# Kernel optimization log

Hardware: AMD Instinct MI355X
Metric: run time of the kernel (lower is better)

The kernel has to match this reference:

```python
import jax, jax.numpy as jnp
import numpy as np

B, S, D, H = 2, 2048, 1024, 16
DEPTH = D // H

def setup_inputs() -> dict:
    key = jax.random.key(0)
    ks = jax.random.split(key, 6)
    sc = 0.02
    return {
        "x": jax.random.normal(ks[0], (B, S, D), dtype=jnp.float32),
        "mask": jnp.ones((S, S), dtype=jnp.int32),
        "wq": jax.random.normal(ks[1], (D, D), dtype=jnp.float32) * sc,
        "bq": jnp.zeros((D,), dtype=jnp.float32),
        "wk": jax.random.normal(ks[2], (D, D), dtype=jnp.float32) * sc,
        "bk": jnp.zeros((D,), dtype=jnp.float32),
        "wv": jax.random.normal(ks[3], (D, D), dtype=jnp.float32) * sc,
        "bv": jnp.zeros((D,), dtype=jnp.float32),
        "wo": jax.random.normal(ks[4], (D, D), dtype=jnp.float32) * sc,
        "bo": jnp.zeros((D,), dtype=jnp.float32),
    }

def _split_heads(t):
    # [B,S,D] -> [B,H,S,depth]
    b, s, _ = t.shape
    return t.reshape(b, s, H, DEPTH).transpose(0, 2, 1, 3)

def reference(x, mask, wq, bq, wk, bk, wv, bv, wo, bo):
    q = _split_heads(x @ wq + bq)
    k = _split_heads(x @ wk + bk)
    v = _split_heads(x @ wv + bv)
    scale = 1.0 / jnp.sqrt(jnp.asarray(DEPTH, x.dtype))
    scores = jnp.einsum('bhqd,bhkd->bhqk', q, k) * scale
    # Faithful to original: band_part(ones,-1,0) is the LOWER triangle
    # (incl. diagonal), and it is ADDED times -1e9 -> lower triangle masked.
    s_len = mask.shape[0]
    tri = jnp.tril(jnp.ones((s_len, s_len), dtype=x.dtype))
    scores = scores + tri * (-1e9)
    attn = jax.nn.softmax(scores, axis=-1)  # dropout is identity at inference
    out = jnp.einsum('bhqk,bhkd->bhqd', attn, v)
    out = out.transpose(0, 2, 1, 3).reshape(x.shape[0], -1, D)
    return out @ wo + bo
```

## Files before the change

### kernel.cpp

```cpp
#include <hip/hip_runtime.h>
#include <hip/hip_bf16.h>


using bf16   = __bf16;
using bf16x2 = __attribute__((ext_vector_type(2))) __bf16;
using bf16x4 = __attribute__((ext_vector_type(4))) __bf16;
using bf16x8 = __attribute__((ext_vector_type(8))) __bf16;
using f32x4  = __attribute__((ext_vector_type(4))) float;
using uintx2 = __attribute__((ext_vector_type(2))) unsigned int;
using uintx4 = __attribute__((ext_vector_type(4))) unsigned int;

#define ATTN_LOG2E 1.4426950408889634f
#define ATTN_MBIAS (-11.541560327111707f)

__device__ __forceinline__ void load_lds16(const void* g, void* l) {
  __builtin_amdgcn_global_load_lds(
      (const __attribute__((address_space(1))) void*)g,
      (__attribute__((address_space(3))) void*)l, 16, 0, 0);
}

__device__ __forceinline__ unsigned int packbf(float a, float b) {
  bf16x2 v;
  v[0] = (bf16)a;
  v[1] = (bf16)b;
  return __builtin_bit_cast(unsigned int, v);
}

__device__ __forceinline__ void xchg_p(unsigned int u, unsigned int v, int hi,
                                       unsigned int& f, unsigned int& s) {
#if __has_builtin(__builtin_amdgcn_permlane32_swap) && \
    __has_builtin(__builtin_amdgcn_permlane16_swap)
  uintx2 ab = __builtin_amdgcn_permlane32_swap(u, v, false, false);
  uintx2 fs = __builtin_amdgcn_permlane16_swap(ab[0], ab[1], false, false);
  f = fs[0];
  s = fs[1];
#else
  unsigned int a = (hi < 2) ? u : (unsigned int)__shfl_xor((int)v, 32);
  unsigned int b = (hi < 2) ? (unsigned int)__shfl_xor((int)u, 32) : v;
  unsigned int a16 = (unsigned int)__shfl_xor((int)a, 16);
  unsigned int b16 = (unsigned int)__shfl_xor((int)b, 16);
  f = (hi & 1) ? b16 : a;
  s = (hi & 1) ? b : a16;
#endif
}

__global__ __launch_bounds__(256) void prep_kernel(
    const float* __restrict__ x, bf16* __restrict__ xb,
    const float* __restrict__ wq, const float* __restrict__ wk,
    const float* __restrict__ wv, const float* __restrict__ wo,
    bf16* __restrict__ wT) {
  const int t = threadIdx.x;
  int bid = blockIdx.x;
  if (bid < 4096) {
    const int i = (bid * 256 + t) * 4;
    const float4 v = *(const float4*)(x + i);
    bf16x4 o;
    o[0] = (bf16)v.x; o[1] = (bf16)v.y; o[2] = (bf16)v.z; o[3] = (bf16)v.w;
    *(bf16x4*)(xb + i) = o;
    return;
  }
  bid -= 4096;
  const int sel = bid >> 8;
  const float* w = (sel == 0) ? wq : (sel == 1) ? wk : (sel == 2) ? wv : wo;
  bf16* out = wT + (size_t)sel * 1048576;
  __shared__ float tile[64][65];
  const int n0 = (bid & 15) * 64;
  const int k0 = ((bid >> 4) & 15) * 64;
#pragma unroll
  for (int p = 0; p < 4; ++p) {
    const int row = p * 16 + (t >> 4);
    const int c4  = (t & 15) * 4;
    const float4 v = *(const float4*)&w[(size_t)(k0 + row) * 1024 + n0 + c4];
    tile[row][c4 + 0] = v.x; tile[row][c4 + 1] = v.y;
    tile[row][c4 + 2] = v.z; tile[row][c4 + 3] = v.w;
  }
  __syncthreads();
#pragma unroll
  for (int p = 0; p < 4; ++p) {
    const int rn = p * 16 + (t >> 4);
    const int c4 = (t & 15) * 4;
    bf16x4 o;
#pragma unroll
    for (int j = 0; j < 4; ++j) o[j] = (bf16)tile[c4 + j][rn];
    *(bf16x4*)&out[(size_t)(n0 + rn) * 1024 + k0 + c4] = o;
  }
}

template <int MODE>
__global__ __launch_bounds__(256, 2) void gemm_bt(
    const bf16* __restrict__ A, const bf16* __restrict__ Bt,
    const float* __restrict__ bias0, const float* __restrict__ bias1,
    const float* __restrict__ bias2, bf16* __restrict__ qf,
    bf16* __restrict__ kfr, bf16* __restrict__ vfr, float* __restrict__ fout,
    int Nblocks) {
  __shared__ __align__(16) char smem[32768];
  char* sA = smem;
  char* sB = smem + 16384;
  const int tid = threadIdx.x;
  const int lane = tid & 63;
  const int w = tid >> 6;
  const int wm = w >> 1, wn = w & 1;
  const int bid = blockIdx.x;
  const int m0 = (bid / Nblocks) * 128;
  const int n0 = (bid % Nblocks) * 128;

  const char* Ab = (const char*)A;
  const char* Bb = (const char*)Bt;
  size_t srcA[4], srcB[4];
#pragma unroll
  for (int it = 0; it < 4; ++it) {
    const int o = it * 4096 + tid * 16;
    const int r = o >> 7;
    const int cg = ((o >> 4) & 7) ^ (r & 7);
    srcA[it] = (size_t)(m0 + r) * 2048 + cg * 16;
    srcB[it] = (size_t)(n0 + r) * 2048 + cg * 16;
  }

  f32x4 acc[4][4] = {};

  for (int kt = 0; kt < 16; ++kt) {
    const size_t kb = (size_t)kt * 128;
#pragma unroll
    for (int it = 0; it < 4; ++it) {
      load_lds16(Ab + srcA[it] + kb, sA + it * 4096 + w * 1024);
      load_lds16(Bb + srcB[it] + kb, sB + it * 4096 + w * 1024);
    }
    asm volatile("s_waitcnt vmcnt(0)" ::: "memory");
    __syncthreads();
#pragma unroll
    for (int ks = 0; ks < 2; ++ks) {
      bf16x8 aF[4], bF[4];
      const int g = (lane >> 4) + 4 * ks;
#pragma unroll
      for (int i = 0; i < 4; ++i) {
        const int ra = wm * 64 + i * 16 + (lane & 15);
        aF[i] = *(const bf16x8*)(sA + ra * 128 + ((g ^ (ra & 7)) << 4));
        const int rb = wn * 64 + i * 16 + (lane & 15);
        bF[i] = *(const bf16x8*)(sB + rb * 128 + ((g ^ (rb & 7)) << 4));
      }
#pragma unroll
      for (int mi = 0; mi < 4; ++mi)
#pragma unroll
        for (int ni = 0; ni < 4; ++ni)
          acc[mi][ni] = __builtin_amdgcn_mfma_f32_16x16x32_bf16(
              aF[mi], bF[ni], acc[mi][ni], 0, 0, 0);
    }
    __syncthreads();
  }

  const int cn = lane & 15;
  const int gq = lane >> 4;
#pragma unroll
  for (int mi = 0; mi < 4; ++mi) {
#pragma unroll
    for (int ni = 0; ni < 4; ++ni) {
      const int n  = n0 + wn * 64 + ni * 16 + cn;
      const int mb = m0 + wm * 64 + mi * 16 + 4 * gq;
      const f32x4 v = acc[mi][ni];
      if (MODE == 0) {
        const float bias =
            (n < 1024) ? bias0[n] : ((n < 2048) ? bias1[n - 1024] : bias2[n - 2048]);
        if (n < 1024) {
#pragma unroll
          for (int j = 0; j < 4; ++j)
            qf[(size_t)(mb + j) * 1024 + n] = (bf16)(v[j] + bias);
        } else if (n < 2048) {
          const int dg = n - 1024;
          const int hh = dg >> 6, d = dg & 63;
          const int ks = d >> 5, hl = (d >> 3) & 3, e = d & 7;
          const int bb = mb >> 11, sl = mb & 2047;
          const int ktt = sl >> 6, tt = (sl >> 4) & 3, ql = sl & 15;
          bf16* dst = kfr +
                      ((((size_t)(bb * 16 + hh) * 32 + ktt) * 4 + tt) * 2 + ks) *
                          512 +
                      (hl * 16 + ql) * 8 + e;
#pragma unroll
          for (int j = 0; j < 4; ++j) dst[j * 8] = (bf16)(v[j] + bias);
        } else {
          const int dg = n - 2048;
          const int hh = dg >> 6, d = dg & 63;
          const int dt = d >> 4, dc = d & 15;
          const int bb = mb >> 11, sl = mb & 2047;
          const int ktt = sl >> 6, ks = (sl >> 5) & 1, hl = (sl >> 3) & 3,
                    e0 = sl & 7;
          bf16x4 pk;
#pragma unroll
          for (int j = 0; j < 4; ++j) pk[j] = (bf16)(v[j] + bias);
          *(bf16x4*)(vfr +
                     ((((size_t)(bb * 16 + hh) * 32 + ktt) * 4 + dt) * 2 + ks) *
                         512 +
                     (hl * 16 + dc) * 8 + e0) = pk;
        }
      } else {
        const float bias = bias0[n];
#pragma unroll
        for (int j = 0; j < 4; ++j)
          fout[(size_t)(mb + j) * 1024 + n] = v[j] + bias;
      }
    }
  }
}

__global__ __launch_bounds__(256, 2) void attn_kernel(
    const bf16* __restrict__ qf, const bf16* __restrict__ kfr,
    const bf16* __restrict__ vfr, bf16* __restrict__ ao,
    bf16* __restrict__ o2buf, float* __restrict__ lbuf) {
  const int tid  = threadIdx.x;
  const int lane = tid & 63;
  const int hi   = lane >> 4;
  const int qlo  = lane & 15;
  const int w    = tid >> 6;
  const int u  = blockIdx.x >> 5;
  const int bh = blockIdx.x & 31;
  const int b = bh >> 4, h = bh & 15;

  const char* kfb = (const char*)kfr + (size_t)bh * 262144 + lane * 16;
  const char* vfb = (const char*)vfr + (size_t)bh * 262144 + lane * 16;
  const char* qbb = (const char*)qf + ((size_t)b * 2048) * 2048 + h * 128;

  bf16x8 onesB;
#pragma unroll
  for (int i = 0; i < 8; ++i) onesB[i] = (bf16)1.0f;

  int nseg, sjq[2], skb[2], ske[2], smode[2];
  if (u < 8) {
    nseg = 1;
    sjq[0] = u; skb[0] = 2 * u; ske[0] = 2 * u + 17; smode[0] = 1;
    sjq[1] = 0; skb[1] = 0; ske[1] = 0; smode[1] = 0;
  } else {
    const int j = u - 8;
    nseg = 2;
    sjq[0] = j;      skb[0] = 2 * j + 17; ske[0] = 32; smode[0] = 2;
    sjq[1] = 15 - j; skb[1] = 30 - 2 * j; ske[1] = 32; smode[1] = 0;
  }

  for (int seg = 0; seg < nseg; ++seg) {
    const int jq = sjq[seg], kbeg = skb[seg], kend = ske[seg];
    const int mode = smode[seg];

    const int q0 = jq * 128;
    const int qb = q0 + w * 32;

    bf16x8 qA[2][2];
#pragma unroll
    for (int nt = 0; nt < 2; ++nt) {
      const char* qrow = qbb + (size_t)(qb + 16 * nt + qlo) * 2048;
#pragma unroll
      for (int ks = 0; ks < 2; ++ks) {
        qA[nt][ks] = *(const bf16x8*)(qrow + ks * 64 + hi * 16);
#pragma unroll
        for (int i = 0; i < 8; ++i)
          qA[nt][ks][i] = (bf16)(0.125f * (float)qA[nt][ks][i]);
      }
    }

    f32x4 lacc[2] = {};
    f32x4 O[2][4] = {};

    bf16x8 kA[2][4], kB[2][4], vF[2][4];

    auto LOADK = [&](int kt, bf16x8 (&kd)[2][4]) {
      const char* kT = kfb + (size_t)kt * 8192;
#pragma unroll
      for (int ks = 0; ks < 2; ++ks)
#pragma unroll
        for (int t = 0; t < 4; ++t)
          kd[ks][t] = *(const bf16x8*)(kT + (t * 2 + ks) * 1024);
    };
    auto LOADV = [&](int kt) {
      const char* vT = vfb + (size_t)kt * 8192;
#pragma unroll
      for (int ks = 0; ks < 2; ++ks)
#pragma unroll
        for (int dt = 0; dt < 4; ++dt)
          vF[ks][dt] = *(const bf16x8*)(vT + (dt * 2 + ks) * 1024);
    };

    auto COMPUTE = [&](int kt, bf16x8 (&kFr)[2][4]) {
      f32x4 sc[2][4] = {};
#pragma unroll
      for (int ks = 0; ks < 2; ++ks)
#pragma unroll
        for (int t = 0; t < 4; ++t) {
          sc[0][t] = __builtin_amdgcn_mfma_f32_16x16x32_bf16(
              kFr[ks][t], qA[0][ks], sc[0][t], 0, 0, 0);
          sc[1][t] = __builtin_amdgcn_mfma_f32_16x16x32_bf16(
              kFr[ks][t], qA[1][ks], sc[1][t], 0, 0, 0);
        }

      if (kt * 64 < q0 + 128) {
        const int k0t = kt * 64;
#pragma unroll
        for (int nt = 0; nt < 2; ++nt)
#pragma unroll
          for (int t = 0; t < 4; ++t)
#pragma unroll
            for (int j = 0; j < 4; ++j) {
              const int kk = k0t + t * 16 + 4 * hi + j;
              const int qq = qb + 16 * nt + qlo;
              if (kk <= qq) sc[nt][t][j] = -1e30f;
            }
      }

#pragma unroll
      for (int nt = 0; nt < 2; ++nt) {
        unsigned int W[4][2];
#pragma unroll
        for (int t = 0; t < 4; ++t)
#pragma unroll
          for (int p = 0; p < 2; ++p)
            W[t][p] = packbf(
                exp2f(fmaf(sc[nt][t][2 * p], ATTN_LOG2E, ATTN_MBIAS)),
                exp2f(fmaf(sc[nt][t][2 * p + 1], ATTN_LOG2E, ATTN_MBIAS)));
#pragma unroll
        for (int ks = 0; ks < 2; ++ks) {
          uintx4 w4;
#pragma unroll
          for (int p = 0; p < 2; ++p) {
            unsigned int f, s;
            xchg_p(W[2 * ks][p], W[2 * ks + 1][p], hi, f, s);
            w4[p] = f;
            w4[2 + p] = s;
          }
          const bf16x8 pA = __builtin_bit_cast(bf16x8, w4);
          lacc[nt] = __builtin_amdgcn_mfma_f32_16x16x32_bf16(pA, onesB,
                                                             lacc[nt], 0, 0, 0);
#pragma unroll
          for (int dt = 0; dt < 4; ++dt)
            O[nt][dt] = __builtin_amdgcn_mfma_f32_16x16x32_bf16(
                pA, vF[ks][dt], O[nt][dt], 0, 0, 0);
        }
      }
    };

    LOADK(kbeg, kA);
    for (int kt = kbeg; kt < kend; kt += 2) {
      LOADV(kt);
      if (kt + 1 < kend) LOADK(kt + 1, kB);
      COMPUTE(kt, kA);
      if (kt + 1 < kend) {
        LOADV(kt + 1);
        if (kt + 2 < kend) LOADK(kt + 2, kA);
        COMPUTE(kt + 1, kB);
      }
    }

    if (mode == 0) {
#pragma unroll
      for (int nt = 0; nt < 2; ++nt)
#pragma unroll
        for (int j = 0; j < 4; ++j) {
          const float linv = (lacc[nt][j] > 0.f) ? 1.f / lacc[nt][j] : 0.f;
          const int qg = qb + 16 * nt + 4 * hi + j;
#pragma unroll
          for (int dt = 0; dt < 4; ++dt)
            ao[(size_t)(b * 2048 + qg) * 1024 + h * 64 + dt * 16 + qlo] =
                (bf16)(O[nt][dt][j] * linv);
        }
    } else {
      const int qtbh = jq * 32 + bh;
      const int slot = mode - 1;
#pragma unroll
      for (int nt = 0; nt < 2; ++nt)
#pragma unroll
        for (int j = 0; j < 4; ++j) {
          const int r = w * 32 + 16 * nt + 4 * hi + j;
#pragma unroll
          for (int dt = 0; dt < 4; ++dt) {
            const bf16 vv = (bf16)O[nt][dt][j];
            if (mode == 1)
              ao[(size_t)(b * 2048 + q0 + r) * 1024 + h * 64 + dt * 16 + qlo] =
                  vv;
            else
              o2buf[(size_t)(qtbh * 128 + r) * 64 + dt * 16 + qlo] = vv;
          }
        }
      if (qlo == 0) {
#pragma unroll
        for (int nt = 0; nt < 2; ++nt)
#pragma unroll
          for (int j = 0; j < 4; ++j)
            lbuf[(qtbh * 2 + slot) * 128 + (w * 32 + 16 * nt + 4 * hi + j)] =
                lacc[nt][j];
      }
    }
  }
}

__global__ __launch_bounds__(256) void combine_kernel(
    const bf16* __restrict__ o2buf, const float* __restrict__ lbuf,
    const bf16* __restrict__ vfr, bf16* __restrict__ ao) {
  const int bid = blockIdx.x;
  if (bid >= 256) {
    const int tid = threadIdx.x;
    const int lane = tid & 63, w = tid >> 6;
    const int gw = (bid - 256) * 4 + w;
    const int bh = gw >> 2, dt = gw & 3;
    const int b = bh >> 4, h = bh & 15;
    const char* vfb = (const char*)vfr + (size_t)bh * 262144 + lane * 16;
    float s = 0.f;
    for (int kt = 0; kt < 32; ++kt) {
#pragma unroll
      for (int ks = 0; ks < 2; ++ks) {
        const bf16x8 v =
            *(const bf16x8*)(vfb + (size_t)kt * 8192 + (dt * 2 + ks) * 1024);
#pragma unroll
        for (int e = 0; e < 8; ++e) s += (float)v[e];
      }
    }
    s += __shfl_xor(s, 16);
    s += __shfl_xor(s, 32);
    if ((lane >> 4) == 0)
      ao[(size_t)(b * 2048 + 2047) * 1024 + h * 64 + dt * 16 + lane] =
          (bf16)(s * (1.f / 2048.f));
    return;
  }

  const int qtbh = bid;
  const int jq = qtbh >> 5, bh = qtbh & 31;
  const int b = bh >> 4, h = bh & 15;
  const int t = threadIdx.x;
  const int r = t >> 1;
  const int c0 = (t & 1) * 32;

  const float l1 = lbuf[(qtbh * 2 + 0) * 128 + r];
  const float l2 = lbuf[(qtbh * 2 + 1) * 128 + r];
  const float denom = l1 + l2;
  const float linv = (denom > 0.f) ? 1.f / denom : 0.f;

  bf16* arow = ao + ((size_t)(b * 2048 + jq * 128 + r) * 1024 + h * 64 + c0);
  const bf16* o2row = o2buf + ((size_t)(qtbh * 128 + r) * 64 + c0);
#pragma unroll
  for (int i = 0; i < 4; ++i) {
    const bf16x8 o1 = *(const bf16x8*)(arow + i * 8);
    const bf16x8 o2 = *(const bf16x8*)(o2row + i * 8);
    bf16x8 o;
#pragma unroll
    for (int j = 0; j < 8; ++j)
      o[j] = (bf16)(((float)o1[j] + (float)o2[j]) * linv);
    *(bf16x8*)(arow + i * 8) = o;
  }
}

extern "C" void kernel_launch(void* const* d_in, const int* in_sizes, int n_in,
                              void* d_out, int out_size, void* d_ws,
                              size_t ws_size, hipStream_t stream) {
  const float* x  = (const float*)d_in[0];
  const float* wq = (const float*)d_in[2];
  const float* bq = (const float*)d_in[3];
  const float* wk = (const float*)d_in[4];
  const float* bk = (const float*)d_in[5];
  const float* wv = (const float*)d_in[6];
  const float* bv = (const float*)d_in[7];
  const float* wo = (const float*)d_in[8];
  const float* bo = (const float*)d_in[9];
  float* out = (float*)d_out;

  if (ws_size < (size_t)25165824 * 2) return;

  bf16* ws    = (bf16*)d_ws;
  bf16* xb    = ws;
  bf16* wqkvT = xb + 4194304;
  bf16* woT   = wqkvT + 3145728;
  bf16* qfp   = woT + 1048576;
  bf16* kfrag = qfp + 4194304;
  bf16* vfrag = kfrag + 4194304;
  bf16* aop   = vfrag + 4194304;

  bf16*  o2buf = xb;
  float* lbuf  = (float*)(xb + 2097152);

  prep_kernel<<<5120, 256, 0, stream>>>(x, xb, wq, wk, wv, wo, wqkvT);

  gemm_bt<0><<<32 * 24, 256, 0, stream>>>(xb, wqkvT, bq, bk, bv, qfp, kfrag,
                                          vfrag, nullptr, 24);
  attn_kernel<<<512, 256, 0, stream>>>(qfp, kfrag, vfrag, aop, o2buf, lbuf);
  combine_kernel<<<288, 256, 0, stream>>>(o2buf, lbuf, vfrag, aop);
  gemm_bt<1><<<32 * 8, 256, 0, stream>>>(aop, woT, bo, nullptr, nullptr, nullptr,
                                         nullptr, nullptr, out, 8);
}
```

Baseline: 108.7 us.

## Split attention key range across two wave groups and reduce through LDS

The attention kernel now runs 512 threads per block: two groups of four waves each process half of the key tiles for the same query rows. The second group writes its partial O and row-sum accumulators to shared memory, and the first group adds them before doing the existing output and partial-result writes. This doubles the parallelism per query tile to hide latency and improve occupancy. In exchange it drops the software double-buffered K/V prefetch, adds a block-wide barrier and an LDS round-trip, and tightens the register budget through the new launch bounds.

```diff
diff --git a/kernel.cpp b/kernel.cpp
--- a/kernel.cpp
+++ b/kernel.cpp
@@ -201,15 +201,19 @@
   }
 }
 
-__global__ __launch_bounds__(256, 2) void attn_kernel(
+__global__ __launch_bounds__(512, 4) void attn_kernel(
     const bf16* __restrict__ qf, const bf16* __restrict__ kfr,
     const bf16* __restrict__ vfr, bf16* __restrict__ ao,
     bf16* __restrict__ o2buf, float* __restrict__ lbuf) {
+  __shared__ __align__(16) char smem[40960];
+
   const int tid  = threadIdx.x;
   const int lane = tid & 63;
   const int hi   = lane >> 4;
   const int qlo  = lane & 15;
-  const int w    = tid >> 6;
+  const int wave = tid >> 6;
+  const int wg   = wave >> 2;
+  const int w    = wave & 3;
   const int u  = blockIdx.x >> 5;
   const int bh = blockIdx.x & 31;
   const int b = bh >> 4, h = bh & 15;
@@ -234,6 +238,8 @@
     sjq[1] = 15 - j; skb[1] = 30 - 2 * j; ske[1] = 32; smode[1] = 0;
   }
 
+  char* const lbase = smem + w * 10240 + lane * 160;
+
   for (int seg = 0; seg < nseg; ++seg) {
     const int jq = sjq[seg], kbeg = skb[seg], kend = ske[seg];
     const int mode = smode[seg];
@@ -257,26 +263,25 @@
     f32x4 lacc[2] = {};
     f32x4 O[2][4] = {};
 
-    bf16x8 kA[2][4], kB[2][4], vF[2][4];
-
-    auto LOADK = [&](int kt, bf16x8 (&kd)[2][4]) {
+    const int half0 = (kend - kbeg + 1) >> 1;
+    const int myb = wg ? (kbeg + half0) : kbeg;
+    const int mye = wg ? kend : (kbeg + half0);
+
+    for (int kt = myb; kt < mye; ++kt) {
       const char* kT = kfb + (size_t)kt * 8192;
+      const char* vT = vfb + (size_t)kt * 8192;
+      bf16x8 kFr[2][4], vF[2][4];
 #pragma unroll
       for (int ks = 0; ks < 2; ++ks)
 #pragma unroll
         for (int t = 0; t < 4; ++t)
-          kd[ks][t] = *(const bf16x8*)(kT + (t * 2 + ks) * 1024);
-    };
-    auto LOADV = [&](int kt) {
-      const char* vT = vfb + (size_t)kt * 8192;
+          kFr[ks][t] = *(const bf16x8*)(kT + (t * 2 + ks) * 1024);
 #pragma unroll
       for (int ks = 0; ks < 2; ++ks)
 #pragma unroll
         for (int dt = 0; dt < 4; ++dt)
           vF[ks][dt] = *(const bf16x8*)(vT + (dt * 2 + ks) * 1024);
-    };
-
-    auto COMPUTE = [&](int kt, bf16x8 (&kFr)[2][4]) {
+
       f32x4 sc[2][4] = {};
 #pragma unroll
       for (int ks = 0; ks < 2; ++ks)
@@ -331,59 +336,76 @@
                 pA, vF[ks][dt], O[nt][dt], 0, 0, 0);
         }
       }
-    };
-
-    LOADK(kbeg, kA);
-    for (int kt = kbeg; kt < kend; kt += 2) {
-      LOADV(kt);
-      if (kt + 1 < kend) LOADK(kt + 1, kB);
-      COMPUTE(kt, kA);
-      if (kt + 1 < kend) {
-        LOADV(kt + 1);
-        if (kt + 2 < kend) LOADK(kt + 2, kA);
-        COMPUTE(kt + 1, kB);
-      }
-    }
-
-    if (mode == 0) {
+    }
+
+    if (wg == 1) {
 #pragma unroll
       for (int nt = 0; nt < 2; ++nt)
 #pragma unroll
-        for (int j = 0; j < 4; ++j) {
-          const float linv = (lacc[nt][j] > 0.f) ? 1.f / lacc[nt][j] : 0.f;
-          const int qg = qb + 16 * nt + 4 * hi + j;
-#pragma unroll
-          for (int dt = 0; dt < 4; ++dt)
-            ao[(size_t)(b * 2048 + qg) * 1024 + h * 64 + dt * 16 + qlo] =
-                (bf16)(O[nt][dt][j] * linv);
+        for (int dt = 0; dt < 4; ++dt)
+          *(f32x4*)(lbase + (nt * 4 + dt) * 16) = O[nt][dt];
+      *(f32x4*)(lbase + 128) = lacc[0];
+      *(f32x4*)(lbase + 144) = lacc[1];
+    }
+    __syncthreads();
+    if (wg == 0) {
+#pragma unroll
+      for (int nt = 0; nt < 2; ++nt)
+#pragma unroll
+        for (int dt = 0; dt < 4; ++dt) {
+          const f32x4 o1 = *(const f32x4*)(lbase + (nt * 4 + dt) * 16);
+#pragma unroll
+          for (int j = 0; j < 4; ++j) O[nt][dt][j] += o1[j];
         }
-    } else {
-      const int qtbh = jq * 32 + bh;
-      const int slot = mode - 1;
-#pragma unroll
-      for (int nt = 0; nt < 2; ++nt)
-#pragma unroll
-        for (int j = 0; j < 4; ++j) {
-          const int r = w * 32 + 16 * nt + 4 * hi + j;
-#pragma unroll
-          for (int dt = 0; dt < 4; ++dt) {
-            const bf16 vv = (bf16)O[nt][dt][j];
-            if (mode == 1)
-              ao[(size_t)(b * 2048 + q0 + r) * 1024 + h * 64 + dt * 16 + qlo] =
-                  vv;
-            else
-              o2buf[(size_t)(qtbh * 128 + r) * 64 + dt * 16 + qlo] = vv;
+      const f32x4 la0 = *(const f32x4*)(lbase + 128);
+      const f32x4 la1 = *(const f32x4*)(lbase + 144);
+#pragma unroll
+      for (int j = 0; j < 4; ++j) {
+        lacc[0][j] += la0[j];
+        lacc[1][j] += la1[j];
+      }
+
+      if (mode == 0) {
+#pragma unroll
+        for (int nt = 0; nt < 2; ++nt)
+#pragma unroll
+          for (int j = 0; j < 4; ++j) {
+            const float linv = (lacc[nt][j] > 0.f) ? 1.f / lacc[nt][j] : 0.f;
+            const int qg = qb + 16 * nt + 4 * hi + j;
+#pragma unroll
+            for (int dt = 0; dt < 4; ++dt)
+              ao[(size_t)(b * 2048 + qg) * 1024 + h * 64 + dt * 16 + qlo] =
+                  (bf16)(O[nt][dt][j] * linv);
           }
+      } else {
+        const int qtbh = jq * 32 + bh;
+        const int slot = mode - 1;
+#pragma unroll
+        for (int nt = 0; nt < 2; ++nt)
+#pragma unroll
+          for (int j = 0; j < 4; ++j) {
+            const int r = w * 32 + 16 * nt + 4 * hi + j;
+#pragma unroll
+            for (int dt = 0; dt < 4; ++dt) {
+              const bf16 vv = (bf16)O[nt][dt][j];
+              if (mode == 1)
+                ao[(size_t)(b * 2048 + q0 + r) * 1024 + h * 64 + dt * 16 +
+                   qlo] = vv;
+              else
+                o2buf[(size_t)(qtbh * 128 + r) * 64 + dt * 16 + qlo] = vv;
+            }
+          }
+        if (qlo == 0) {
+#pragma unroll
+          for (int nt = 0; nt < 2; ++nt)
+#pragma unroll
+            for (int j = 0; j < 4; ++j)
+              lbuf[(qtbh * 2 + slot) * 128 +
+                   (w * 32 + 16 * nt + 4 * hi + j)] = lacc[nt][j];
         }
-      if (qlo == 0) {
-#pragma unroll
-        for (int nt = 0; nt < 2; ++nt)
-#pragma unroll
-          for (int j = 0; j < 4; ++j)
-            lbuf[(qtbh * 2 + slot) * 128 + (w * 32 + 16 * nt + 4 * hi + j)] =
-                lacc[nt][j];
-      }
-    }
+      }
+    }
+    __syncthreads();
   }
 }
 
@@ -474,7 +496,7 @@
 
   gemm_bt<0><<<32 * 24, 256, 0, stream>>>(xb, wqkvT, bq, bk, bv, qfp, kfrag,
                                           vfrag, nullptr, 24);
-  attn_kernel<<<512, 256, 0, stream>>>(qfp, kfrag, vfrag, aop, o2buf, lbuf);
+  attn_kernel<<<512, 512, 0, stream>>>(qfp, kfrag, vfrag, aop, o2buf, lbuf);
   combine_kernel<<<288, 256, 0, stream>>>(o2buf, lbuf, vfrag, aop);
   gemm_bt<1><<<32 * 8, 256, 0, stream>>>(aop, woT, bo, nullptr, nullptr, nullptr,
                                          nullptr, nullptr, out, 8);
```

After: 142.3 us. 1.31x slower.

## Rewrite QKV projection GEMM with 256x256 tiles, double-buffered LDS and XOR swizzle

Applied to the files above, without the earlier changes.

Replaces the templated 128x128 QKV GEMM with a dedicated kernel using 512 threads, 256x256 output tiles, a BK=64 double-buffered LDS pipeline via global_load_lds, and an XOR-swizzled LDS layout. Block indices are remapped so neighbouring blocks share operand tiles. The larger tiles raise arithmetic intensity and cut redundant global loads, and the prefetch overlaps loads with MFMA work. In exchange it uses 128KB of LDS and many accumulator registers, and launches only 192 blocks, which may leave some of the 256 compute units idle.

```diff
diff --git a/kernel.cpp b/kernel.cpp
--- a/kernel.cpp
+++ b/kernel.cpp
@@ -86,13 +86,148 @@
   }
 }
 
-template <int MODE>
-__global__ __launch_bounds__(256, 2) void gemm_bt(
+__global__ __launch_bounds__(512, 2) void gemm_qkv(
     const bf16* __restrict__ A, const bf16* __restrict__ Bt,
     const float* __restrict__ bias0, const float* __restrict__ bias1,
     const float* __restrict__ bias2, bf16* __restrict__ qf,
-    bf16* __restrict__ kfr, bf16* __restrict__ vfr, float* __restrict__ fout,
-    int Nblocks) {
+    bf16* __restrict__ kfr, bf16* __restrict__ vfr) {
+  __shared__ __align__(16) char smem[131072];
+  char* const sAb = smem;
+  char* const sBb = smem + 65536;
+
+  const int tid  = threadIdx.x;
+  const int lane = tid & 63;
+  const int qlo  = lane & 15;
+  const int hi   = lane >> 4;
+  const int wv   = tid >> 6;
+  const int wm   = wv >> 2;
+  const int wn   = wv & 3;
+
+  const int swz = (blockIdx.x & 7) * 24 + (blockIdx.x >> 3);
+  const int m0 = (swz / 12) * 256;
+  const int n0 = (swz % 12) * 256;
+
+  const char* Ab = (const char*)A;
+  const char* Bb = (const char*)Bt;
+
+  const int r_  = tid >> 3;
+  const int cg_ = (tid & 7) ^ (r_ & 7);
+  size_t srcA[4], srcB[4];
+#pragma unroll
+  for (int i = 0; i < 4; ++i) {
+    srcA[i] = (size_t)(m0 + i * 64 + r_) * 2048 + cg_ * 16;
+    srcB[i] = (size_t)(n0 + i * 64 + r_) * 2048 + cg_ * 16;
+  }
+
+  f32x4 acc[8][4] = {};
+
+  auto STAGE = [&](int kt, int buf) {
+    const size_t kb = (size_t)kt * 128;
+    char* dA = sAb + buf * 32768 + wv * 1024;
+    char* dB = sBb + buf * 32768 + wv * 1024;
+#pragma unroll
+    for (int i = 0; i < 4; ++i) {
+      load_lds16(Ab + srcA[i] + kb, dA + i * 8192);
+      load_lds16(Bb + srcB[i] + kb, dB + i * 8192);
+    }
+  };
+
+  STAGE(0, 0);
+  asm volatile("s_waitcnt vmcnt(0)" ::: "memory");
+  __syncthreads();
+
+  for (int kt = 0; kt < 16; ++kt) {
+    const int cur = kt & 1;
+    if (kt + 1 < 16) STAGE(kt + 1, cur ^ 1);
+
+    const char* bA = sAb + cur * 32768;
+    const char* bB = sBb + cur * 32768;
+
+    bf16x8 bF[4][2];
+#pragma unroll
+    for (int ni = 0; ni < 4; ++ni)
+#pragma unroll
+      for (int kk = 0; kk < 2; ++kk) {
+        const int rb = wn * 64 + ni * 16 + qlo;
+        const int g = kk * 4 + hi;
+        bF[ni][kk] = *(const bf16x8*)(bB + rb * 128 + ((g ^ (rb & 7)) << 4));
+      }
+
+#pragma unroll
+    for (int half = 0; half < 2; ++half) {
+      bf16x8 aF[4][2];
+#pragma unroll
+      for (int mi2 = 0; mi2 < 4; ++mi2)
+#pragma unroll
+        for (int kk = 0; kk < 2; ++kk) {
+          const int ra = wm * 128 + (half * 4 + mi2) * 16 + qlo;
+          const int g = kk * 4 + hi;
+          aF[mi2][kk] =
+              *(const bf16x8*)(bA + ra * 128 + ((g ^ (ra & 7)) << 4));
+        }
+#pragma unroll
+      for (int mi2 = 0; mi2 < 4; ++mi2)
+#pragma unroll
+        for (int ni = 0; ni < 4; ++ni)
+#pragma unroll
+          for (int kk = 0; kk < 2; ++kk)
+            acc[half * 4 + mi2][ni] = __builtin_amdgcn_mfma_f32_16x16x32_bf16(
+                aF[mi2][kk], bF[ni][kk], acc[half * 4 + mi2][ni], 0, 0, 0);
+    }
+
+    if (kt + 1 < 16) {
+      asm volatile("s_waitcnt vmcnt(0)" ::: "memory");
+      __syncthreads();
+    }
+  }
+
+#pragma unroll
+  for (int mi = 0; mi < 8; ++mi) {
+#pragma unroll
+    for (int ni = 0; ni < 4; ++ni) {
+      const int n  = n0 + wn * 64 + ni * 16 + qlo;
+      const int mb = m0 + wm * 128 + mi * 16 + 4 * hi;
+      const f32x4 v = acc[mi][ni];
+      const float bias =
+          (n < 1024) ? bias0[n] : ((n < 2048) ? bias1[n - 1024] : bias2[n - 2048]);
+      if (n < 1024) {
+#pragma unroll
+        for (int j = 0; j < 4; ++j)
+          qf[(size_t)(mb + j) * 1024 + n] = (bf16)(v[j] + bias);
+      } else if (n < 2048) {
+        const int dg = n - 1024;
+        const int hh = dg >> 6, d = dg & 63;
+        const int ks = d >> 5, hl = (d >> 3) & 3, e = d & 7;
+        const int bb = mb >> 11, sl = mb & 2047;
+        const int ktt = sl >> 6, tt = (sl >> 4) & 3, ql = sl & 15;
+        bf16* dst = kfr +
+                    ((((size_t)(bb * 16 + hh) * 32 + ktt) * 4 + tt) * 2 + ks) *
+                        512 +
+                    (hl * 16 + ql) * 8 + e;
+#pragma unroll
+        for (int j = 0; j < 4; ++j) dst[j * 8] = (bf16)(v[j] + bias);
+      } else {
+        const int dg = n - 2048;
+        const int hh = dg >> 6, d = dg & 63;
+        const int dt = d >> 4, dc = d & 15;
+        const int bb = mb >> 11, sl = mb & 2047;
+        const int ktt = sl >> 6, ks = (sl >> 5) & 1, hl = (sl >> 3) & 3,
+                  e0 = sl & 7;
+        bf16x4 pk;
+#pragma unroll
+        for (int j = 0; j < 4; ++j) pk[j] = (bf16)(v[j] + bias);
+        *(bf16x4*)(vfr +
+                   ((((size_t)(bb * 16 + hh) * 32 + ktt) * 4 + dt) * 2 + ks) *
+                       512 +
+                   (hl * 16 + dc) * 8 + e0) = pk;
+      }
+    }
+  }
+}
+
+__global__ __launch_bounds__(256, 2) void gemm_out(
+    const bf16* __restrict__ A, const bf16* __restrict__ Bt,
+    const float* __restrict__ bias0, float* __restrict__ fout, int Nblocks) {
   __shared__ __align__(16) char smem[32768];
   char* sA = smem;
   char* sB = smem + 16384;
@@ -157,46 +292,10 @@
       const int n  = n0 + wn * 64 + ni * 16 + cn;
       const int mb = m0 + wm * 64 + mi * 16 + 4 * gq;
       const f32x4 v = acc[mi][ni];
-      if (MODE == 0) {
-        const float bias =
-            (n < 1024) ? bias0[n] : ((n < 2048) ? bias1[n - 1024] : bias2[n - 2048]);
-        if (n < 1024) {
-#pragma unroll
-          for (int j = 0; j < 4; ++j)
-            qf[(size_t)(mb + j) * 1024 + n] = (bf16)(v[j] + bias);
-        } else if (n < 2048) {
-          const int dg = n - 1024;
-          const int hh = dg >> 6, d = dg & 63;
-          const int ks = d >> 5, hl = (d >> 3) & 3, e = d & 7;
-          const int bb = mb >> 11, sl = mb & 2047;
-          const int ktt = sl >> 6, tt = (sl >> 4) & 3, ql = sl & 15;
-          bf16* dst = kfr +
-                      ((((size_t)(bb * 16 + hh) * 32 + ktt) * 4 + tt) * 2 + ks) *
-                          512 +
-                      (hl * 16 + ql) * 8 + e;
-#pragma unroll
-          for (int j = 0; j < 4; ++j) dst[j * 8] = (bf16)(v[j] + bias);
-        } else {
-          const int dg = n - 2048;
-          const int hh = dg >> 6, d = dg & 63;
-          const int dt = d >> 4, dc = d & 15;
-          const int bb = mb >> 11, sl = mb & 2047;
-          const int ktt = sl >> 6, ks = (sl >> 5) & 1, hl = (sl >> 3) & 3,
-                    e0 = sl & 7;
-          bf16x4 pk;
-#pragma unroll
-          for (int j = 0; j < 4; ++j) pk[j] = (bf16)(v[j] + bias);
-          *(bf16x4*)(vfr +
-                     ((((size_t)(bb * 16 + hh) * 32 + ktt) * 4 + dt) * 2 + ks) *
-                         512 +
-                     (hl * 16 + dc) * 8 + e0) = pk;
-        }
-      } else {
-        const float bias = bias0[n];
-#pragma unroll
-        for (int j = 0; j < 4; ++j)
-          fout[(size_t)(mb + j) * 1024 + n] = v[j] + bias;
-      }
+      const float bias = bias0[n];
+#pragma unroll
+      for (int j = 0; j < 4; ++j)
+        fout[(size_t)(mb + j) * 1024 + n] = v[j] + bias;
     }
   }
 }
@@ -472,10 +571,8 @@
 
   prep_kernel<<<5120, 256, 0, stream>>>(x, xb, wq, wk, wv, wo, wqkvT);
 
-  gemm_bt<0><<<32 * 24, 256, 0, stream>>>(xb, wqkvT, bq, bk, bv, qfp, kfrag,
-                                          vfrag, nullptr, 24);
+  gemm_qkv<<<192, 512, 0, stream>>>(xb, wqkvT, bq, bk, bv, qfp, kfrag, vfrag);
   attn_kernel<<<512, 256, 0, stream>>>(qfp, kfrag, vfrag, aop, o2buf, lbuf);
   combine_kernel<<<288, 256, 0, stream>>>(o2buf, lbuf, vfrag, aop);
-  gemm_bt<1><<<32 * 8, 256, 0, stream>>>(aop, woT, bo, nullptr, nullptr, nullptr,
-                                         nullptr, nullptr, out, 8);
-}
+  gemm_out<<<32 * 8, 256, 0, stream>>>(aop, woT, bo, out, 8);
+}
```

Measured after the change: 111.6 us. 1.03x slower.

## Split attention key ranges into table-driven chunks across more blocks

Applied to the files above, without the earlier changes.

Replaces the two-segment-per-block causal work split with a 36-entry chunk table, so each of 1152 blocks handles one query tile over a bounded key range (up to three partial slots per tile, combined later). This aims to balance work across CUs and raise the block count. Occupancy bounds go from 2 to 4 blocks per CU, and the manual double-buffered K prefetch is dropped in favour of a simple load-then-compute loop. In exchange the combine kernel reads three partial buffers for some tiles, and the lost prefetch may expose load latency.

```diff
diff --git a/kernel.cpp b/kernel.cpp
--- a/kernel.cpp
+++ b/kernel.cpp
@@ -43,6 +43,44 @@
   s = (hi & 1) ? b : a16;
 #endif
 }
+
+__device__ const unsigned int kChunkTab[36] = {
+    0u  | (0u << 8)  | (11u << 16) | (0u << 24),
+    0u  | (11u << 8) | (22u << 16) | (1u << 24),
+    0u  | (22u << 8) | (32u << 16) | (2u << 24),
+    1u  | (2u << 8)  | (12u << 16) | (0u << 24),
+    1u  | (12u << 8) | (22u << 16) | (1u << 24),
+    1u  | (22u << 8) | (32u << 16) | (2u << 24),
+    2u  | (4u << 8)  | (14u << 16) | (0u << 24),
+    2u  | (14u << 8) | (23u << 16) | (1u << 24),
+    2u  | (23u << 8) | (32u << 16) | (2u << 24),
+    3u  | (6u << 8)  | (15u << 16) | (0u << 24),
+    3u  | (15u << 8) | (24u << 16) | (1u << 24),
+    4u  | (8u << 8)  | (16u << 16) | (0u << 24),
+    4u  | (16u << 8) | (24u << 16) | (1u << 24),
+    4u  | (24u << 8) | (32u << 16) | (2u << 24),
+    8u  | (16u << 8) | (24u << 16) | (0u << 24),
+    8u  | (24u << 8) | (32u << 16) | (1u << 24),
+    12u | (24u << 8) | (32u << 16) | (3u << 24),
+    3u  | (24u << 8) | (32u << 16) | (2u << 24),
+    5u  | (10u << 8) | (18u << 16) | (0u << 24),
+    5u  | (18u << 8) | (25u << 16) | (1u << 24),
+    5u  | (25u << 8) | (32u << 16) | (2u << 24),
+    6u  | (12u << 8) | (19u << 16) | (0u << 24),
+    6u  | (19u << 8) | (26u << 16) | (1u << 24),
+    9u  | (18u << 8) | (25u << 16) | (0u << 24),
+    9u  | (25u << 8) | (32u << 16) | (1u << 24),
+    6u  | (26u << 8) | (32u << 16) | (2u << 24),
+    7u  | (14u << 8) | (20u << 16) | (0u << 24),
+    7u  | (20u << 8) | (26u << 16) | (1u << 24),
+    7u  | (26u << 8) | (32u << 16) | (2u << 24),
+    10u | (20u << 8) | (26u << 16) | (0u << 24),
+    10u | (26u << 8) | (32u << 16) | (1u << 24),
+    13u | (26u << 8) | (32u << 16) | (3u << 24),
+    11u | (22u << 8) | (27u << 16) | (0u << 24),
+    11u | (27u << 8) | (32u << 16) | (1u << 24),
+    14u | (28u << 8) | (32u << 16) | (3u << 24),
+    15u | (30u << 8) | (32u << 16) | (3u << 24)};
 
 __global__ __launch_bounds__(256) void prep_kernel(
     const float* __restrict__ x, bf16* __restrict__ xb,
@@ -201,10 +239,11 @@
   }
 }
 
-__global__ __launch_bounds__(256, 2) void attn_kernel(
+__global__ __launch_bounds__(256, 4) void attn_kernel(
     const bf16* __restrict__ qf, const bf16* __restrict__ kfr,
     const bf16* __restrict__ vfr, bf16* __restrict__ ao,
-    bf16* __restrict__ o2buf, float* __restrict__ lbuf) {
+    bf16* __restrict__ sc1, bf16* __restrict__ sc2,
+    float* __restrict__ lbuf) {
   const int tid  = threadIdx.x;
   const int lane = tid & 63;
   const int hi   = lane >> 4;
@@ -214,6 +253,10 @@
   const int bh = blockIdx.x & 31;
   const int b = bh >> 4, h = bh & 15;
 
+  const unsigned int ent = kChunkTab[u];
+  const int jq = ent & 255, kbeg = (ent >> 8) & 255, kend = (ent >> 16) & 255;
+  const int slot = ent >> 24;
+
   const char* kfb = (const char*)kfr + (size_t)bh * 262144 + lane * 16;
   const char* vfb = (const char*)vfr + (size_t)bh * 262144 + lane * 16;
   const char* qbb = (const char*)qf + ((size_t)b * 2048) * 2048 + h * 128;
@@ -222,179 +265,147 @@
 #pragma unroll
   for (int i = 0; i < 8; ++i) onesB[i] = (bf16)1.0f;
 
-  int nseg, sjq[2], skb[2], ske[2], smode[2];
-  if (u < 8) {
-    nseg = 1;
-    sjq[0] = u; skb[0] = 2 * u; ske[0] = 2 * u + 17; smode[0] = 1;
-    sjq[1] = 0; skb[1] = 0; ske[1] = 0; smode[1] = 0;
+  const int q0 = jq * 128;
+  const int qb = q0 + w * 32;
+
+  bf16x8 qA[2][2];
+#pragma unroll
+  for (int nt = 0; nt < 2; ++nt) {
+    const char* qrow = qbb + (size_t)(qb + 16 * nt + qlo) * 2048;
+#pragma unroll
+    for (int ks = 0; ks < 2; ++ks) {
+      qA[nt][ks] = *(const bf16x8*)(qrow + ks * 64 + hi * 16);
+#pragma unroll
+      for (int i = 0; i < 8; ++i)
+        qA[nt][ks][i] = (bf16)(0.125f * (float)qA[nt][ks][i]);
+    }
+  }
+
+  f32x4 lacc[2] = {};
+  f32x4 O[2][4] = {};
+
+  for (int kt = kbeg; kt < kend; ++kt) {
+    const char* kT = kfb + (size_t)kt * 8192;
+    const char* vT = vfb + (size_t)kt * 8192;
+    bf16x8 kFr[2][4], vF[2][4];
+#pragma unroll
+    for (int ks = 0; ks < 2; ++ks)
+#pragma unroll
+      for (int t = 0; t < 4; ++t)
+        kFr[ks][t] = *(const bf16x8*)(kT + (t * 2 + ks) * 1024);
+#pragma unroll
+    for (int ks = 0; ks < 2; ++ks)
+#pragma unroll
+      for (int dt = 0; dt < 4; ++dt)
+        vF[ks][dt] = *(const bf16x8*)(vT + (dt * 2 + ks) * 1024);
+
+    f32x4 sc[2][4] = {};
+#pragma unroll
+    for (int ks = 0; ks < 2; ++ks)
+#pragma unroll
+      for (int t = 0; t < 4; ++t) {
+        sc[0][t] = __builtin_amdgcn_mfma_f32_16x16x32_bf16(
+            kFr[ks][t], qA[0][ks], sc[0][t], 0, 0, 0);
+        sc[1][t] = __builtin_amdgcn_mfma_f32_16x16x32_bf16(
+            kFr[ks][t], qA[1][ks], sc[1][t], 0, 0, 0);
+      }
+
+    if (kt * 64 < q0 + 128) {
+      const int k0t = kt * 64;
+#pragma unroll
+      for (int nt = 0; nt < 2; ++nt)
+#pragma unroll
+        for (int t = 0; t < 4; ++t)
+#pragma unroll
+          for (int j = 0; j < 4; ++j) {
+            const int kk = k0t + t * 16 + 4 * hi + j;
+            const int qq = qb + 16 * nt + qlo;
+            if (kk <= qq) sc[nt][t][j] = -1e30f;
+          }
+    }
+
+#pragma unroll
+    for (int nt = 0; nt < 2; ++nt) {
+      unsigned int W[4][2];
+#pragma unroll
+      for (int t = 0; t < 4; ++t)
+#pragma unroll
+        for (int p = 0; p < 2; ++p)
+          W[t][p] = packbf(
+              exp2f(fmaf(sc[nt][t][2 * p], ATTN_LOG2E, ATTN_MBIAS)),
+              exp2f(fmaf(sc[nt][t][2 * p + 1], ATTN_LOG2E, ATTN_MBIAS)));
+#pragma unroll
+      for (int ks = 0; ks < 2; ++ks) {
+        uintx4 w4;
+#pragma unroll
+        for (int p = 0; p < 2; ++p) {
+          unsigned int f, s;
+          xchg_p(W[2 * ks][p], W[2 * ks + 1][p], hi, f, s);
+          w4[p] = f;
+          w4[2 + p] = s;
+        }
+        const bf16x8 pA = __builtin_bit_cast(bf16x8, w4);
+        lacc[nt] = __builtin_amdgcn_mfma_f32_16x16x32_bf16(pA, onesB, lacc[nt],
+                                                           0, 0, 0);
+#pragma unroll
+        for (int dt = 0; dt < 4; ++dt)
+          O[nt][dt] = __builtin_amdgcn_mfma_f32_16x16x32_bf16(
+              pA, vF[ks][dt], O[nt][dt], 0, 0, 0);
+      }
+    }
+  }
+
+  if (slot == 3) {
+#pragma unroll
+    for (int nt = 0; nt < 2; ++nt)
+#pragma unroll
+      for (int j = 0; j < 4; ++j) {
+        const float linv = (lacc[nt][j] > 0.f) ? 1.f / lacc[nt][j] : 0.f;
+        const int qg = qb + 16 * nt + 4 * hi + j;
+#pragma unroll
+        for (int dt = 0; dt < 4; ++dt)
+          ao[(size_t)(b * 2048 + qg) * 1024 + h * 64 + dt * 16 + qlo] =
+              (bf16)(O[nt][dt][j] * linv);
+      }
   } else {
-    const int j = u - 8;
-    nseg = 2;
-    sjq[0] = j;      skb[0] = 2 * j + 17; ske[0] = 32; smode[0] = 2;
-    sjq[1] = 15 - j; skb[1] = 30 - 2 * j; ske[1] = 32; smode[1] = 0;
-  }
-
-  for (int seg = 0; seg < nseg; ++seg) {
-    const int jq = sjq[seg], kbeg = skb[seg], kend = ske[seg];
-    const int mode = smode[seg];
-
-    const int q0 = jq * 128;
-    const int qb = q0 + w * 32;
-
-    bf16x8 qA[2][2];
-#pragma unroll
-    for (int nt = 0; nt < 2; ++nt) {
-      const char* qrow = qbb + (size_t)(qb + 16 * nt + qlo) * 2048;
-#pragma unroll
-      for (int ks = 0; ks < 2; ++ks) {
-        qA[nt][ks] = *(const bf16x8*)(qrow + ks * 64 + hi * 16);
-#pragma unroll
-        for (int i = 0; i < 8; ++i)
-          qA[nt][ks][i] = (bf16)(0.125f * (float)qA[nt][ks][i]);
-      }
-    }
-
-    f32x4 lacc[2] = {};
-    f32x4 O[2][4] = {};
-
-    bf16x8 kA[2][4], kB[2][4], vF[2][4];
-
-    auto LOADK = [&](int kt, bf16x8 (&kd)[2][4]) {
-      const char* kT = kfb + (size_t)kt * 8192;
-#pragma unroll
-      for (int ks = 0; ks < 2; ++ks)
-#pragma unroll
-        for (int t = 0; t < 4; ++t)
-          kd[ks][t] = *(const bf16x8*)(kT + (t * 2 + ks) * 1024);
-    };
-    auto LOADV = [&](int kt) {
-      const char* vT = vfb + (size_t)kt * 8192;
-#pragma unroll
-      for (int ks = 0; ks < 2; ++ks)
-#pragma unroll
-        for (int dt = 0; dt < 4; ++dt)
-          vF[ks][dt] = *(const bf16x8*)(vT + (dt * 2 + ks) * 1024);
-    };
-
-    auto COMPUTE = [&](int kt, bf16x8 (&kFr)[2][4]) {
-      f32x4 sc[2][4] = {};
-#pragma unroll
-      for (int ks = 0; ks < 2; ++ks)
-#pragma unroll
-        for (int t = 0; t < 4; ++t) {
-          sc[0][t] = __builtin_amdgcn_mfma_f32_16x16x32_bf16(
-              kFr[ks][t], qA[0][ks], sc[0][t], 0, 0, 0);
-          sc[1][t] = __builtin_amdgcn_mfma_f32_16x16x32_bf16(
-              kFr[ks][t], qA[1][ks], sc[1][t], 0, 0, 0);
-        }
-
-      if (kt * 64 < q0 + 128) {
-        const int k0t = kt * 64;
-#pragma unroll
-        for (int nt = 0; nt < 2; ++nt)
-#pragma unroll
-          for (int t = 0; t < 4; ++t)
-#pragma unroll
-            for (int j = 0; j < 4; ++j) {
-              const int kk = k0t + t * 16 + 4 * hi + j;
-              const int qq = qb + 16 * nt + qlo;
-              if (kk <= qq) sc[nt][t][j] = -1e30f;
-            }
-      }
-
-#pragma unroll
-      for (int nt = 0; nt < 2; ++nt) {
-        unsigned int W[4][2];
-#pragma unroll
-        for (int t = 0; t < 4; ++t)
-#pragma unroll
-          for (int p = 0; p < 2; ++p)
-            W[t][p] = packbf(
-                exp2f(fmaf(sc[nt][t][2 * p], ATTN_LOG2E, ATTN_MBIAS)),
-                exp2f(fmaf(sc[nt][t][2 * p + 1], ATTN_LOG2E, ATTN_MBIAS)));
-#pragma unroll
-        for (int ks = 0; ks < 2; ++ks) {
-          uintx4 w4;
-#pragma unroll
-          for (int p = 0; p < 2; ++p) {
-            unsigned int f, s;
-            xchg_p(W[2 * ks][p], W[2 * ks + 1][p], hi, f, s);
-            w4[p] = f;
-            w4[2 + p] = s;
-          }
-          const bf16x8 pA = __builtin_bit_cast(bf16x8, w4);
-          lacc[nt] = __builtin_amdgcn_mfma_f32_16x16x32_bf16(pA, onesB,
-                                                             lacc[nt], 0, 0, 0);
-#pragma unroll
-          for (int dt = 0; dt < 4; ++dt)
-            O[nt][dt] = __builtin_amdgcn_mfma_f32_16x16x32_bf16(
-                pA, vF[ks][dt], O[nt][dt], 0, 0, 0);
-        }
-      }
-    };
-
-    LOADK(kbeg, kA);
-    for (int kt = kbeg; kt < kend; kt += 2) {
-      LOADV(kt);
-      if (kt + 1 < kend) LOADK(kt + 1, kB);
-      COMPUTE(kt, kA);
-      if (kt + 1 < kend) {
-        LOADV(kt + 1);
-        if (kt + 2 < kend) LOADK(kt + 2, kA);
-        COMPUTE(kt + 1, kB);
-      }
-    }
-
-    if (mode == 0) {
-#pragma unroll
-      for (int nt = 0; nt < 2; ++nt)
-#pragma unroll
-        for (int j = 0; j < 4; ++j) {
-          const float linv = (lacc[nt][j] > 0.f) ? 1.f / lacc[nt][j] : 0.f;
-          const int qg = qb + 16 * nt + 4 * hi + j;
-#pragma unroll
-          for (int dt = 0; dt < 4; ++dt)
-            ao[(size_t)(b * 2048 + qg) * 1024 + h * 64 + dt * 16 + qlo] =
-                (bf16)(O[nt][dt][j] * linv);
-        }
-    } else {
-      const int qtbh = jq * 32 + bh;
-      const int slot = mode - 1;
-#pragma unroll
-      for (int nt = 0; nt < 2; ++nt)
-#pragma unroll
-        for (int j = 0; j < 4; ++j) {
-          const int r = w * 32 + 16 * nt + 4 * hi + j;
-#pragma unroll
-          for (int dt = 0; dt < 4; ++dt) {
-            const bf16 vv = (bf16)O[nt][dt][j];
-            if (mode == 1)
-              ao[(size_t)(b * 2048 + q0 + r) * 1024 + h * 64 + dt * 16 + qlo] =
-                  vv;
-            else
-              o2buf[(size_t)(qtbh * 128 + r) * 64 + dt * 16 + qlo] = vv;
+    const int qtbh = jq * 32 + bh;
+#pragma unroll
+    for (int nt = 0; nt < 2; ++nt)
+#pragma unroll
+      for (int j = 0; j < 4; ++j) {
+        const int r = w * 32 + 16 * nt + 4 * hi + j;
+#pragma unroll
+        for (int dt = 0; dt < 4; ++dt) {
+          const bf16 vv = (bf16)O[nt][dt][j];
+          if (slot == 0)
+            ao[(size_t)(b * 2048 + q0 + r) * 1024 + h * 64 + dt * 16 + qlo] =
+                vv;
+          else {
+            bf16* sc_ = (slot == 1) ? sc1 : sc2;
+            sc_[(size_t)(qtbh * 128 + r) * 64 + dt * 16 + qlo] = vv;
           }
         }
-      if (qlo == 0) {
-#pragma unroll
-        for (int nt = 0; nt < 2; ++nt)
-#pragma unroll
-          for (int j = 0; j < 4; ++j)
-            lbuf[(qtbh * 2 + slot) * 128 + (w * 32 + 16 * nt + 4 * hi + j)] =
-                lacc[nt][j];
-      }
+      }
+    if (qlo == 0) {
+#pragma unroll
+      for (int nt = 0; nt < 2; ++nt)
+#pragma unroll
+        for (int j = 0; j < 4; ++j)
+          lbuf[slot * 49152 + qtbh * 128 + (w * 32 + 16 * nt + 4 * hi + j)] =
+              lacc[nt][j];
     }
   }
 }
 
 __global__ __launch_bounds__(256) void combine_kernel(
-    const bf16* __restrict__ o2buf, const float* __restrict__ lbuf,
-    const bf16* __restrict__ vfr, bf16* __restrict__ ao) {
+    const bf16* __restrict__ sc1, const bf16* __restrict__ sc2,
+    const float* __restrict__ lbuf, const bf16* __restrict__ vfr,
+    bf16* __restrict__ ao) {
   const int bid = blockIdx.x;
-  if (bid >= 256) {
+  if (bid >= 384) {
     const int tid = threadIdx.x;
     const int lane = tid & 63, w = tid >> 6;
-    const int gw = (bid - 256) * 4 + w;
+    const int gw = (bid - 384) * 4 + w;
     const int bh = gw >> 2, dt = gw & 3;
     const int b = bh >> 4, h = bh & 15;
     const char* vfb = (const char*)vfr + (size_t)bh * 262144 + lane * 16;
@@ -422,22 +433,28 @@
   const int t = threadIdx.x;
   const int r = t >> 1;
   const int c0 = (t & 1) * 32;
-
-  const float l1 = lbuf[(qtbh * 2 + 0) * 128 + r];
-  const float l2 = lbuf[(qtbh * 2 + 1) * 128 + r];
-  const float denom = l1 + l2;
-  const float linv = (denom > 0.f) ? 1.f / denom : 0.f;
+  const bool three = (jq < 8);
+
+  float l = lbuf[qtbh * 128 + r] + lbuf[49152 + qtbh * 128 + r];
+  if (three) l += lbuf[98304 + qtbh * 128 + r];
+  const float linv = (l > 0.f) ? 1.f / l : 0.f;
 
   bf16* arow = ao + ((size_t)(b * 2048 + jq * 128 + r) * 1024 + h * 64 + c0);
-  const bf16* o2row = o2buf + ((size_t)(qtbh * 128 + r) * 64 + c0);
+  const bf16* s1row = sc1 + ((size_t)(qtbh * 128 + r) * 64 + c0);
+  const bf16* s2row = sc2 + ((size_t)(qtbh * 128 + r) * 64 + c0);
 #pragma unroll
   for (int i = 0; i < 4; ++i) {
-    const bf16x8 o1 = *(const bf16x8*)(arow + i * 8);
-    const bf16x8 o2 = *(const bf16x8*)(o2row + i * 8);
+    const bf16x8 o0 = *(const bf16x8*)(arow + i * 8);
+    const bf16x8 o1 = *(const bf16x8*)(s1row + i * 8);
+    bf16x8 o2;
+    if (three) o2 = *(const bf16x8*)(s2row + i * 8);
     bf16x8 o;
 #pragma unroll
-    for (int j = 0; j < 8; ++j)
-      o[j] = (bf16)(((float)o1[j] + (float)o2[j]) * linv);
+    for (int j = 0; j < 8; ++j) {
+      float acc = (float)o0[j] + (float)o1[j];
+      if (three) acc += (float)o2[j];
+      o[j] = (bf16)(acc * linv);
+    }
     *(bf16x8*)(arow + i * 8) = o;
   }
 }
@@ -467,15 +484,16 @@
   bf16* vfrag = kfrag + 4194304;
   bf16* aop   = vfrag + 4194304;
 
-  bf16*  o2buf = xb;
-  float* lbuf  = (float*)(xb + 2097152);
+  bf16*  sc1  = xb;
+  float* lbuf = (float*)(xb + 3145728);
+  bf16*  sc2  = wqkvT;
 
   prep_kernel<<<5120, 256, 0, stream>>>(x, xb, wq, wk, wv, wo, wqkvT);
 
   gemm_bt<0><<<32 * 24, 256, 0, stream>>>(xb, wqkvT, bq, bk, bv, qfp, kfrag,
                                           vfrag, nullptr, 24);
-  attn_kernel<<<512, 256, 0, stream>>>(qfp, kfrag, vfrag, aop, o2buf, lbuf);
-  combine_kernel<<<288, 256, 0, stream>>>(o2buf, lbuf, vfrag, aop);
-  gemm_bt<1><<<32 * 8, 256, 0, stream>>>(aop, woT, bo, nullptr, nullptr, nullptr,
-                                         nullptr, nullptr, out, 8);
-}
+  attn_kernel<<<1152, 256, 0, stream>>>(qfp, kfrag, vfrag, aop, sc1, sc2, lbuf);
+  combine_kernel<<<416, 256, 0, stream>>>(sc1, sc2, lbuf, vfrag, aop);
+  gemm_bt<1><<<32 * 8, 256, 0, stream>>>(aop, woT, bo, nullptr, nullptr,
+                                         nullptr, nullptr, nullptr, out, 8);
+}
```

After: 150.9 us. 38.7% more time.
